# Kernel optimization log

Measured on AMD Instinct MI355X. Metric: run time of the kernel, lower is better.

The kernel has to match this reference:

```python
import jax, jax.numpy as jnp
import numpy as np

# Genotype (DARTS RNN): 8 recurrent steps (activation, predecessor index) + concat indices
GENO = [("relu", 0), ("relu", 1), ("tanh", 2), ("relu", 3),
        ("relu", 4), ("identity", 1), ("relu", 5), ("relu", 1)]
CONCAT = [1, 2, 3, 4, 5, 6, 7, 8]
NINP, NHID = 256, 256
T, B = 1024, 64
INITRANGE = 0.04

_ACT = {"tanh": jnp.tanh, "relu": jax.nn.relu,
        "sigmoid": jax.nn.sigmoid, "identity": lambda v: v}


def setup_inputs() -> dict:
    key = jax.random.key(0)
    k1, k2, k3, k4 = jax.random.split(key, 4)
    inputs = jax.random.normal(k1, (T, B, NINP), dtype=jnp.float32)
    hidden = jax.random.normal(k2, (1, B, NHID), dtype=jnp.float32)
    W0 = jax.random.uniform(k3, (NINP + NHID, 2 * NHID), dtype=jnp.float32,
                            minval=-INITRANGE, maxval=INITRANGE)
    Ws = jax.random.uniform(k4, (len(GENO), NHID, 2 * NHID), dtype=jnp.float32,
                            minval=-INITRANGE, maxval=INITRANGE)
    return {"inputs": inputs, "hidden": hidden, "W0": W0, "Ws": Ws}


def _cell(x, h_prev, W0, Ws):
    # init state: s0 = h_prev + sigmoid(c0) * (tanh(h0) - h_prev)
    xh = jnp.concatenate([x, h_prev], axis=-1)          # [B, ninp+nhid]
    c0, h0 = jnp.split(xh @ W0, 2, axis=-1)             # each [B, nhid]
    s0 = h_prev + jax.nn.sigmoid(c0) * (jnp.tanh(h0) - h_prev)
    states = [s0]
    for i, (name, pred) in enumerate(GENO):
        s_prev = states[pred]
        c, h = jnp.split(s_prev @ Ws[i], 2, axis=-1)
        states.append(s_prev + jax.nn.sigmoid(c) * (_ACT[name](h) - s_prev))
    return jnp.mean(jnp.stack([states[i] for i in CONCAT], axis=-1), axis=-1)


def reference(inputs, hidden, W0, Ws):
    h0 = hidden[0]  # [B, nhid]

    def step(h, x):
        h_new = _cell(x, h, W0, Ws)
        return h_new, h_new

    _, hiddens = jax.lax.scan(step, h0, inputs)  # [T, B, nhid]
    return hiddens, hiddens[-1][None]
```

## Files before the change

kernel.cpp:

```cpp
#include <hip/hip_runtime.h>


#define TT 1024
#define NWG 16

typedef __attribute__((ext_vector_type(8))) short bf16x8;
typedef __attribute__((ext_vector_type(4))) float f32x4;
typedef __attribute__((ext_vector_type(2))) unsigned int u32x2;

__device__ __forceinline__ unsigned short f2bf(float f) {
  unsigned u = __builtin_bit_cast(unsigned, f);
  u += 0x7FFFu + ((u >> 16) & 1u);
  return (unsigned short)(u >> 16);
}
__device__ __forceinline__ float sigm(float c) { return 1.0f / (1.0f + __expf(-c)); }
__device__ __forceinline__ float tanh_f(float h) {
  float e = __expf(2.0f * h);
  return 1.0f - 2.0f / (e + 1.0f);
}

__device__ __forceinline__ void lda_sc(bf16x8& r, const void* p) {
  asm volatile("global_load_dwordx4 %0, %1, off sc0 sc1" : "=v"(r) : "v"(p));
}
#define ASM_WAIT8(A) asm volatile("s_waitcnt vmcnt(0)" \
  : "+v"((A)[0]), "+v"((A)[1]), "+v"((A)[2]), "+v"((A)[3]), \
    "+v"((A)[4]), "+v"((A)[5]), "+v"((A)[6]), "+v"((A)[7]) :: "memory")

__global__ void darts_init(const float* __restrict__ hid,
                           unsigned short* __restrict__ sf,
                           unsigned* __restrict__ flags) {
  int tid = blockIdx.x * 256 + threadIdx.x;
  if (tid < 512) flags[tid] = 0;
  int lane = tid & 63, mt = (tid >> 6) & 3, kc = tid >> 8;
  const float* ph = hid + (mt * 16 + (lane & 15)) * 256 + kc * 32 + (lane >> 4) * 8;
  bf16x8 v;
#pragma unroll
  for (int e = 0; e < 8; ++e) v[e] = (short)f2bf(ph[e]);
  *(bf16x8*)(sf + 6 * 16384 + tid * 8) = v;
}

__global__ void __launch_bounds__(256, 1) darts_main(
    const float* __restrict__ x, const float* __restrict__ hid,
    const float* __restrict__ W0g, const float* __restrict__ Wsg,
    float* __restrict__ out,
    unsigned short* __restrict__ sf, unsigned* __restrict__ flags) {
  extern __shared__ char sm[];
  const int wg = blockIdx.x, tid = threadIdx.x;
  const int wv = tid >> 6;
  const int lane = tid & 63;

  for (int c = 0; c < 32; ++c) {
    int flat = tid + 256 * c;
    int fl = flat & 63, kc = (flat >> 6) & 7, n = (flat >> 9) & 1, gi = flat >> 10;
    int col = n * 256 + wg * 16 + (fl & 15);
    int kb = kc * 32 + (fl >> 4) * 8;
    bf16x8 v;
#pragma unroll
    for (int e = 0; e < 8; ++e) v[e] = (short)f2bf(Wsg[(gi * 256 + kb + e) * 512 + col]);
    *(bf16x8*)(&sm[flat * 16]) = v;
  }

  bf16x8 w0c[16], w0h[16];
#pragma unroll
  for (int kc = 0; kc < 16; ++kc) {
    int kb = kc * 32 + (lane >> 4) * 8;
    bf16x8 vc, vh;
#pragma unroll
    for (int e = 0; e < 8; ++e) {
      vc[e] = (short)f2bf(W0g[(kb + e) * 512 + wg * 16 + (lane & 15)]);
      vh[e] = (short)f2bf(W0g[(kb + e) * 512 + 256 + wg * 16 + (lane & 15)]);
    }
    w0c[kc] = vc; w0h[kc] = vh;
  }

  const int m = wv * 16 + (lane & 15);
  const int n0 = wg * 16 + (lane >> 4) * 4;

  float hprev[4];
  float st[9][4];
  {
    f32x4 h4 = *(const f32x4*)(hid + m * 256 + n0);
#pragma unroll
    for (int r = 0; r < 4; ++r) hprev[r] = h4[r];
  }

  const int wbase = ((((wg >> 1) * 4 + wv) * 64 +
                      (lane & 15) + 16 * ((wg * 2 + (lane >> 5)) & 3)) * 8) +
                    ((lane >> 4) & 1) * 4;

  __syncthreads();

  unsigned short* sfh = sf + 6 * 16384;
  float* const outp = out + (size_t)m * 256 + n0;

#define PUBLISH(TOK) do { \
    unsigned tk_ = (unsigned)(TOK); \
    asm volatile("s_waitcnt vmcnt(0)" ::: "memory"); \
    __syncthreads(); \
    if (tid == 0) \
      asm volatile("global_store_dword %0, %1, off sc0 sc1" \
                   :: "v"(flags + wg), "v"(tk_) : "memory"); \
  } while (0)

#define POLL(TOK) do { \
    unsigned tk_ = (unsigned)(TOK); \
    if (tk_) { unsigned fv_; \
      do { \
        asm volatile("global_load_dword %0, %1, off sc0 sc1\n\t" \
                     "s_waitcnt vmcnt(0)" \
                     : "=v"(fv_) : "v"(flags + (lane & 15)) : "memory"); \
      } while (__any((int)(fv_ < tk_))); \
    } \
  } while (0)

#define GBAR(TOK) do { PUBLISH(TOK); POLL(TOK); } while (0)

#define LOADA(BUF) do { _Pragma("unroll") \
    for (int kc = 0; kc < 8; ++kc) \
      lda_sc(a[kc], (const unsigned short*)(BUF) + ((kc * 4 + wv) * 64 + lane) * 8); \
    ASM_WAIT8(a); \
  } while (0)

#define MM(GI, AC, AH) do { _Pragma("unroll") \
    for (int kc = 0; kc < 8; ++kc) { \
      bf16x8 bc = *(const bf16x8*)(&sm[((((GI) * 2 + 0) * 8 + kc) * 64 + lane) * 16]); \
      bf16x8 bh = *(const bf16x8*)(&sm[((((GI) * 2 + 1) * 8 + kc) * 64 + lane) * 16]); \
      AC = __builtin_amdgcn_mfma_f32_16x16x32_bf16(bc, a[kc], AC, 0, 0, 0); \
      AH = __builtin_amdgcn_mfma_f32_16x16x32_bf16(bh, a[kc], AH, 0, 0, 0); \
    } } while (0)

#define UPD(SI, PR, ACT, AC, AH) do { _Pragma("unroll") \
    for (int r = 0; r < 4; ++r) { \
      float g = sigm((AC)[r]); float hh = (AH)[r]; \
      float av = (ACT) == 0 ? fmaxf(hh, 0.0f) : ((ACT) == 1 ? tanh_f(hh) : hh); \
      st[SI][r] = st[PR][r] + g * (av - st[PR][r]); \
    } } while (0)

#define STOREF(BUF, SI) do { \
    unsigned lo_ = (unsigned)f2bf(st[SI][0]) | ((unsigned)f2bf(st[SI][1]) << 16); \
    unsigned hi_ = (unsigned)f2bf(st[SI][2]) | ((unsigned)f2bf(st[SI][3]) << 16); \
    u32x2 v_; v_[0] = lo_; v_[1] = hi_; \
    asm volatile("global_store_dwordx2 %0, %1, off sc0 sc1" \
                 :: "v"((unsigned short*)(BUF) + wbase), "v"(v_) : "memory"); \
  } while (0)

#pragma clang loop unroll(disable)
  for (int t = 0; t < TT; ++t) {
    f32x4 c0 = {0, 0, 0, 0}, h0 = {0, 0, 0, 0};
    {
      bf16x8 ax[8];
#pragma unroll
      for (int kc = 0; kc < 8; ++kc) {
        const float* px = x + ((t * 64 + m) * 256 + kc * 32 + (lane >> 4) * 8);
        bf16x8 v;
#pragma unroll
        for (int e = 0; e < 8; ++e) v[e] = (short)f2bf(px[e]);
        ax[kc] = v;
      }
#pragma unroll
      for (int kc = 0; kc < 8; ++kc) {
        c0 = __builtin_amdgcn_mfma_f32_16x16x32_bf16(w0c[kc], ax[kc], c0, 0, 0, 0);
        h0 = __builtin_amdgcn_mfma_f32_16x16x32_bf16(w0h[kc], ax[kc], h0, 0, 0, 0);
      }
    }
    POLL(t * 7);
    {
      bf16x8 ahf[8];
#pragma unroll
      for (int kc = 0; kc < 8; ++kc)
        lda_sc(ahf[kc], sfh + ((kc * 4 + wv) * 64 + lane) * 8);
      ASM_WAIT8(ahf);
#pragma unroll
      for (int kc = 0; kc < 8; ++kc) {
        c0 = __builtin_amdgcn_mfma_f32_16x16x32_bf16(w0c[8 + kc], ahf[kc], c0, 0, 0, 0);
        h0 = __builtin_amdgcn_mfma_f32_16x16x32_bf16(w0h[8 + kc], ahf[kc], h0, 0, 0, 0);
      }
#pragma unroll
      for (int r = 0; r < 4; ++r) {
        float g = sigm(c0[r]);
        float th = tanh_f(h0[r]);
        st[0][r] = hprev[r] + g * (th - hprev[r]);
      }
      STOREF(sf + 0 * 16384, 0);
    }
    GBAR(t * 7 + 1);

    bf16x8 a[8];
    {
      LOADA(sf + 0 * 16384);
      f32x4 ac = {0, 0, 0, 0}, ah = {0, 0, 0, 0};
      MM(0, ac, ah);
      UPD(1, 0, 0, ac, ah);
      STOREF(sf + 1 * 16384, 1);
    }
    GBAR(t * 7 + 2);
    {
      LOADA(sf + 1 * 16384);
      f32x4 c2 = {0, 0, 0, 0}, h2 = {0, 0, 0, 0};
      MM(1, c2, h2);
      UPD(2, 1, 0, c2, h2);
      STOREF(sf + 2 * 16384, 2);
      PUBLISH(t * 7 + 3);
      f32x4 c6 = {0, 0, 0, 0}, h6 = {0, 0, 0, 0}, c8 = {0, 0, 0, 0}, h8 = {0, 0, 0, 0};
      MM(5, c6, h6); MM(7, c8, h8);
      UPD(6, 1, 2, c6, h6);
      UPD(8, 1, 0, c8, h8);
      POLL(t * 7 + 3);
    }
    {
      LOADA(sf + 2 * 16384);
      f32x4 ac = {0, 0, 0, 0}, ah = {0, 0, 0, 0};
      MM(2, ac, ah);
      UPD(3, 2, 1, ac, ah);
      STOREF(sf + 3 * 16384, 3);
    }
    GBAR(t * 7 + 4);
    {
      LOADA(sf + 3 * 16384);
      f32x4 ac = {0, 0, 0, 0}, ah = {0, 0, 0, 0};
      MM(3, ac, ah);
      UPD(4, 3, 0, ac, ah);
      STOREF(sf + 4 * 16384, 4);
    }
    GBAR(t * 7 + 5);
    {
      LOADA(sf + 4 * 16384);
      f32x4 ac = {0, 0, 0, 0}, ah = {0, 0, 0, 0};
      MM(4, ac, ah);
      UPD(5, 4, 0, ac, ah);
      STOREF(sf + 5 * 16384, 5);
    }
    GBAR(t * 7 + 6);
    {
      LOADA(sf + 5 * 16384);
      f32x4 ac = {0, 0, 0, 0}, ah = {0, 0, 0, 0};
      MM(6, ac, ah);
      UPD(7, 5, 0, ac, ah);
      float hv[4];
#pragma unroll
      for (int r = 0; r < 4; ++r) {
        hv[r] = (st[1][r] + st[2][r] + st[3][r] + st[4][r] +
                 st[5][r] + st[6][r] + st[7][r] + st[8][r]) * 0.125f;
        hprev[r] = hv[r];
      }
      {
        unsigned lo_ = (unsigned)f2bf(hv[0]) | ((unsigned)f2bf(hv[1]) << 16);
        unsigned hi_ = (unsigned)f2bf(hv[2]) | ((unsigned)f2bf(hv[3]) << 16);
        u32x2 v_; v_[0] = lo_; v_[1] = hi_;
        asm volatile("global_store_dwordx2 %0, %1, off sc0 sc1"
                     :: "v"(sfh + wbase), "v"(v_) : "memory");
      }
      PUBLISH(t * 7 + 7);
      f32x4 o4 = {hv[0], hv[1], hv[2], hv[3]};
      *(f32x4*)(outp + (size_t)t * 16384) = o4;
      if (t == TT - 1) *(f32x4*)(out + 16777216 + (size_t)m * 256 + n0) = o4;
    }
  }
#undef PUBLISH
#undef POLL
#undef GBAR
#undef LOADA
#undef MM
#undef UPD
#undef STOREF
}

extern "C" void kernel_launch(void* const* d_in, const int* in_sizes, int n_in,
                              void* d_out, int out_size, void* d_ws, size_t ws_size,
                              hipStream_t stream) {
  const float* x   = (const float*)d_in[0];
  const float* hid = (const float*)d_in[1];
  const float* W0  = (const float*)d_in[2];
  const float* Ws  = (const float*)d_in[3];
  float* out = (float*)d_out;
  unsigned short* sf = (unsigned short*)d_ws;
  unsigned* flags = (unsigned*)((char*)d_ws + 7 * 32768);

  hipFuncSetAttribute((const void*)darts_main,
                      hipFuncAttributeMaxDynamicSharedMemorySize, 131072);
  darts_init<<<8, 256, 0, stream>>>(hid, sf, flags);
  darts_main<<<NWG, 256, 131072, stream>>>(x, hid, W0, Ws, out, sf, flags);
}
```

Before: 20.54 ms.

## Use per-wave flags and pipelined polling for the cross-workgroup barrier

The grid barrier moves from one flag per workgroup to one flag per wave. This works because each wave only consumes the batch rows that the matching wave in the other workgroups produces, so the __syncthreads in PUBLISH can be dropped. Polling now keeps four flag loads in flight and checks them in rotation with vmcnt(3), which shortens the time to notice a flag update. The cost is a flags array four times larger and more memory traffic while spinning. It also relies on the flag region being sized and zeroed for 64 entries.

```diff
diff --git a/kernel.cpp b/kernel.cpp
--- a/kernel.cpp
+++ b/kernel.cpp
@@ -91,25 +91,39 @@
   __syncthreads();
 
   unsigned short* sfh = sf + 6 * 16384;
+  unsigned* const myflag = flags + (wv * 16 + wg);
+  const unsigned* const pollp = flags + (wv * 16 + (lane & 15));
   float* const outp = out + (size_t)m * 256 + n0;
+
+  unsigned pf0 = 0, pf1 = 0, pf2 = 0, pf3 = 0;
+
+#define POLL_FENCE() asm volatile("" : "+v"(pf0), "+v"(pf1), "+v"(pf2), "+v"(pf3))
 
 #define PUBLISH(TOK) do { \
     unsigned tk_ = (unsigned)(TOK); \
     asm volatile("s_waitcnt vmcnt(0)" ::: "memory"); \
-    __syncthreads(); \
-    if (tid == 0) \
+    if (lane == 0) \
       asm volatile("global_store_dword %0, %1, off sc0 sc1" \
-                   :: "v"(flags + wg), "v"(tk_) : "memory"); \
+                   :: "v"(myflag), "v"(tk_) : "memory"); \
   } while (0)
+
+#define POLL_STEP(F) \
+    asm volatile("s_waitcnt vmcnt(3)" : "+v"(F) :: "memory"); \
+    if (!__any((int)((F) < tk_))) break; \
+    asm volatile("global_load_dword %0, %1, off sc0 sc1" : "=&v"(F) : "v"(pollp));
 
 #define POLL(TOK) do { \
     unsigned tk_ = (unsigned)(TOK); \
-    if (tk_) { unsigned fv_; \
-      do { \
-        asm volatile("global_load_dword %0, %1, off sc0 sc1\n\t" \
-                     "s_waitcnt vmcnt(0)" \
-                     : "=v"(fv_) : "v"(flags + (lane & 15)) : "memory"); \
-      } while (__any((int)(fv_ < tk_))); \
+    if (tk_) { \
+      asm volatile( \
+        "global_load_dword %0, %4, off sc0 sc1\n\t" \
+        "global_load_dword %1, %4, off sc0 sc1\n\t" \
+        "global_load_dword %2, %4, off sc0 sc1\n\t" \
+        "global_load_dword %3, %4, off sc0 sc1" \
+        : "=&v"(pf0), "=&v"(pf1), "=&v"(pf2), "=&v"(pf3) : "v"(pollp)); \
+      for (;;) { \
+        POLL_STEP(pf0) POLL_STEP(pf1) POLL_STEP(pf2) POLL_STEP(pf3) \
+      } \
     } \
   } while (0)
 
@@ -119,6 +133,7 @@
     for (int kc = 0; kc < 8; ++kc) \
       lda_sc(a[kc], (const unsigned short*)(BUF) + ((kc * 4 + wv) * 64 + lane) * 8); \
     ASM_WAIT8(a); \
+    POLL_FENCE(); \
   } while (0)
 
 #define MM(GI, AC, AH) do { _Pragma("unroll") \
@@ -170,6 +185,7 @@
       for (int kc = 0; kc < 8; ++kc)
         lda_sc(ahf[kc], sfh + ((kc * 4 + wv) * 64 + lane) * 8);
       ASM_WAIT8(ahf);
+      POLL_FENCE();
 #pragma unroll
       for (int kc = 0; kc < 8; ++kc) {
         c0 = __builtin_amdgcn_mfma_f32_16x16x32_bf16(w0c[8 + kc], ahf[kc], c0, 0, 0, 0);
@@ -256,7 +272,9 @@
       if (t == TT - 1) *(f32x4*)(out + 16777216 + (size_t)m * 256 + n0) = o4;
     }
   }
+#undef POLL_FENCE
 #undef PUBLISH
+#undef POLL_STEP
 #undef POLL
 #undef GBAR
 #undef LOADA
```

Result: slower. 30.87 ms (+50.3%).
